# Kernel tuning notes

Measured on AMD Instinct MI355X. Metric: run time of the kernel, lower is better.

## Reference

```python
import jax, jax.numpy as jnp
import numpy as np

B, S, D = 2, 2048, 1024
H, DK, DV = 16, 64, 64
NEG = -1e9

def setup_inputs() -> dict:
    key = jax.random.key(0)
    ks = jax.random.split(key, 7)
    scale = 1.0 / np.sqrt(D)
    return {
        "Q": jax.random.normal(ks[0], (B, S, D), dtype=jnp.float32),
        "K": jax.random.normal(ks[1], (B, S, D), dtype=jnp.float32),
        "V": jax.random.normal(ks[2], (B, S, D), dtype=jnp.float32),
        "Wq": jax.random.normal(ks[3], (D, H * DK), dtype=jnp.float32) * scale,
        "Wk": jax.random.normal(ks[4], (D, H * DK), dtype=jnp.float32) * scale,
        "Wv": jax.random.normal(ks[5], (D, H * DV), dtype=jnp.float32) * scale,
        "Wo": jax.random.normal(ks[6], (H * DV, D), dtype=jnp.float32) * scale,
    }

def reference(Q, K, V, Wq, Wk, Wv, Wo):
    b, sq, _ = Q.shape
    sk = K.shape[1]
    # project and split heads: [b, h, s, d]
    q = (Q @ Wq).reshape(b, sq, H, DK).transpose(0, 2, 1, 3)
    k = (K @ Wk).reshape(b, sk, H, DK).transpose(0, 2, 1, 3)
    v = (V @ Wv).reshape(b, sk, H, DV).transpose(0, 2, 1, 3)
    scores = jnp.einsum("bhqd,bhkd->bhqk", q, k) / jnp.sqrt(jnp.float32(DK))
    causal = jnp.tril(jnp.ones((sq, sk), dtype=bool))
    scores = jnp.where(causal[None, None], scores, NEG)
    attn = jax.nn.softmax(scores, axis=-1)
    out = jnp.einsum("bhqk,bhkd->bhqd", attn, v)
    out = out.transpose(0, 2, 1, 3).reshape(b, sq, H * DV)
    return out @ Wo
```

## Files before the change

kernel.cpp:

```cpp
#include <hip/hip_runtime.h>
#include <cstdint>
#include <cstddef>


typedef __bf16 bf16x8 __attribute__((ext_vector_type(8)));
typedef __bf16 bf16x4 __attribute__((ext_vector_type(4)));
typedef float f32x4 __attribute__((ext_vector_type(4)));
typedef unsigned int u32x4 __attribute__((ext_vector_type(4)));

#define MFMA __builtin_amdgcn_mfma_f32_16x16x32_bf16

static __device__ __forceinline__ __bf16 f2b(float f) { return (__bf16)f; }

__global__ __launch_bounds__(256) void wtrans_kernel(
    const float* __restrict__ w0, const float* __restrict__ w1,
    const float* __restrict__ w2, const float* __restrict__ w3,
    __bf16* __restrict__ outT)
{
  const int z = blockIdx.z;
  const float* W = (z == 0) ? w0 : (z == 1) ? w1 : (z == 2) ? w2 : w3;
  __bf16* O = outT + (size_t)z * 1048576;
  __shared__ float t[32][33];
  const int tx = threadIdx.x & 31, ty = threadIdx.x >> 5;
  const int kb = blockIdx.y * 32, nb = blockIdx.x * 32;
#pragma unroll
  for (int i = 0; i < 4; i++)
    t[ty + i * 8][tx] = W[(size_t)(kb + ty + i * 8) * 1024 + nb + tx];
  __syncthreads();
#pragma unroll
  for (int i = 0; i < 4; i++)
    O[(size_t)(nb + ty + i * 8) * 1024 + kb + tx] = f2b(t[tx][ty + i * 8]);
}

__global__ __launch_bounds__(256) void gemm_proj_kernel(
    const float* __restrict__ A0, const float* __restrict__ A1,
    const float* __restrict__ A2, const __bf16* __restrict__ WT,
    __bf16* __restrict__ C0, __bf16* __restrict__ C1, __bf16* __restrict__ C2)
{
  const int z = blockIdx.y;
  const float* A = (z == 0) ? A0 : (z == 1) ? A1 : A2;
  const __bf16* W = WT + (size_t)z * 1048576;
  __bf16* C = (z == 0) ? C0 : (z == 1) ? C1 : C2;

  const int mt = blockIdx.x >> 3, nt = blockIdx.x & 7;
  const int mbase = mt * 128, nbase = nt * 128;

  __shared__ __align__(16) __bf16 As[128][40];
  __shared__ __align__(16) __bf16 Bs[128][40];

  const int tid = threadIdx.x;
  const int wid = tid >> 6, lane = tid & 63;
  const int wr = wid >> 1, wc = wid & 1;
  const int lr = lane & 15, kg = lane >> 4;

  f32x4 acc[4][4] = {};

  const int arow = tid >> 3, ac0 = (tid & 7) * 4;

  for (int kb = 0; kb < 32; ++kb) {
    const int k0 = kb * 32;
#pragma unroll
    for (int p = 0; p < 4; ++p) {
      const int r = arow + p * 32;
      f32x4 av = *(const f32x4*)&A[(size_t)(mbase + r) * 1024 + k0 + ac0];
      bf16x4 cv = {f2b(av[0]), f2b(av[1]), f2b(av[2]), f2b(av[3])};
      *(bf16x4*)&As[r][ac0] = cv;
    }
#pragma unroll
    for (int p = 0; p < 2; ++p) {
      const int idx = p * 256 + tid;
      const int r = idx >> 2, c8 = (idx & 3) * 8;
      *(u32x4*)&Bs[r][c8] = *(const u32x4*)&W[(size_t)(nbase + r) * 1024 + k0 + c8];
    }
    __syncthreads();

    bf16x8 af[4], bfr[4];
#pragma unroll
    for (int i = 0; i < 4; i++) af[i] = *(const bf16x8*)&As[wr * 64 + i * 16 + lr][kg * 8];
#pragma unroll
    for (int j = 0; j < 4; j++) bfr[j] = *(const bf16x8*)&Bs[wc * 64 + j * 16 + lr][kg * 8];
#pragma unroll
    for (int i = 0; i < 4; i++)
#pragma unroll
      for (int j = 0; j < 4; j++)
        acc[i][j] = MFMA(af[i], bfr[j], acc[i][j], 0, 0, 0);
    __syncthreads();
  }

  if (z == 2) {
#pragma unroll
    for (int i = 0; i < 4; i++)
#pragma unroll
      for (int j = 0; j < 4; j++) {
        const int m0 = mbase + wr * 64 + i * 16 + kg * 4;
        const int n = nbase + wc * 64 + j * 16 + lr;
        const int b = m0 >> 11, s = m0 & 2047, h = n >> 6, dv = n & 63;
        bf16x4 w;
#pragma unroll
        for (int r = 0; r < 4; r++) w[r] = f2b(acc[i][j][r]);
        *(bf16x4*)&C[(((size_t)(b * 16 + h)) * 64 + dv) * 2048 + s] = w;
      }
  } else {
#pragma unroll
    for (int i = 0; i < 4; i++)
#pragma unroll
      for (int j = 0; j < 4; j++)
#pragma unroll
        for (int r = 0; r < 4; r++) {
          const int m = mbase + wr * 64 + i * 16 + kg * 4 + r;
          const int n = nbase + wc * 64 + j * 16 + lr;
          const int b = m >> 11, s = m & 2047, h = n >> 6, dk = n & 63;
          C[(((size_t)(b * 16 + h)) * 2048 + s) * 64 + dk] = f2b(acc[i][j][r]);
        }
  }
}

__global__ __launch_bounds__(256) void attn_kernel(
    const __bf16* __restrict__ Qh, const __bf16* __restrict__ Kh,
    const __bf16* __restrict__ VTh, __bf16* __restrict__ AO)
{
  const int lin = blockIdx.y * 16 + blockIdx.x;
  const int l = (lin & 7) * 64 + (lin >> 3);
  const int xp = l & 15, bh = l >> 4;
  const int b = bh >> 4, h = bh & 15;
  const __bf16* Qp = Qh + (size_t)bh * 2048 * 64;
  const __bf16* Kp = Kh + (size_t)bh * 2048 * 64;
  const __bf16* Vp = VTh + (size_t)bh * 64 * 2048;

  __shared__ __align__(16) __bf16 Ks[2][64][72];
  __shared__ __align__(16) __bf16 Vt[2][64][72];
  __shared__ __align__(16) __bf16 Ps[4][16][72];

  const int tid = threadIdx.x, wid = tid >> 6, lane = tid & 63;
  const int lr = lane & 15, kg = lane >> 4;
  const int sr0 = tid >> 3, sc0 = (tid & 7) * 8;
  const float SCALE = 0.125f * 1.44269504f;

#pragma unroll
  for (int phase = 0; phase < 2; ++phase) {
    const int qblk = phase ? (31 - xp) : xp;
    const int qbase = qblk << 6;
    const int nkv = qblk + 1;
    const int wq = qbase + wid * 16;

    bf16x8 qf0 = *(const bf16x8*)&Qp[(size_t)(wq + lr) * 64 + kg * 8];
    bf16x8 qf1 = *(const bf16x8*)&Qp[(size_t)(wq + lr) * 64 + 32 + kg * 8];

    f32x4 ot[4] = {};
    float mrow = -1e30f, lsum = 0.f;

    u32x4 kr0 = *(const u32x4*)&Kp[(size_t)sr0 * 64 + sc0];
    u32x4 kr1 = *(const u32x4*)&Kp[(size_t)(sr0 + 32) * 64 + sc0];
    u32x4 vr0 = *(const u32x4*)&Vp[(size_t)sr0 * 2048 + sc0];
    u32x4 vr1 = *(const u32x4*)&Vp[(size_t)(sr0 + 32) * 2048 + sc0];
    __syncthreads();
    *(u32x4*)&Ks[0][sr0][sc0] = kr0;
    *(u32x4*)&Ks[0][sr0 + 32][sc0] = kr1;
    *(u32x4*)&Vt[0][sr0][sc0] = vr0;
    *(u32x4*)&Vt[0][sr0 + 32][sc0] = vr1;

    int cur = 0;
    for (int t = 0; t < nkv; ++t) {
      const int kv0 = t << 6;
      const bool pre = (t + 1 < nkv);
      if (pre) {
        const int nkv0 = kv0 + 64;
        kr0 = *(const u32x4*)&Kp[(size_t)(nkv0 + sr0) * 64 + sc0];
        kr1 = *(const u32x4*)&Kp[(size_t)(nkv0 + sr0 + 32) * 64 + sc0];
        vr0 = *(const u32x4*)&Vp[(size_t)sr0 * 2048 + nkv0 + sc0];
        vr1 = *(const u32x4*)&Vp[(size_t)(sr0 + 32) * 2048 + nkv0 + sc0];
      }
      __syncthreads();

      if (kv0 <= wq + 15) {
        f32x4 st[4] = {};
        __builtin_amdgcn_s_setprio(1);
#pragma unroll
        for (int kvt = 0; kvt < 4; ++kvt) {
          bf16x8 kf0 = *(const bf16x8*)&Ks[cur][kvt * 16 + lr][kg * 8];
          bf16x8 kf1 = *(const bf16x8*)&Ks[cur][kvt * 16 + lr][32 + kg * 8];
          st[kvt] = MFMA(kf0, qf0, st[kvt], 0, 0, 0);
          st[kvt] = MFMA(kf1, qf1, st[kvt], 0, 0, 0);
        }
        __builtin_amdgcn_s_setprio(0);

        const int qidx = wq + lr;
        const bool needmask = (kv0 + 63) > wq;
        float sv[16];
        float mx = -1e30f;
#pragma unroll
        for (int kvt = 0; kvt < 4; ++kvt)
#pragma unroll
          for (int r = 0; r < 4; ++r) {
            float v = st[kvt][r] * SCALE;
            if (needmask && (kv0 + kvt * 16 + kg * 4 + r > qidx)) v = -1e30f;
            sv[kvt * 4 + r] = v;
            mx = fmaxf(mx, v);
          }
        mx = fmaxf(mx, __shfl_xor(mx, 16));
        mx = fmaxf(mx, __shfl_xor(mx, 32));
        const float mnew = fmaxf(mrow, mx);
        const float scl = exp2f(mrow - mnew);
        mrow = mnew;
        float rs = 0.f;
#pragma unroll
        for (int kvt = 0; kvt < 4; ++kvt) {
          bf16x4 pk;
#pragma unroll
          for (int r = 0; r < 4; ++r) {
            const float p = exp2f(sv[kvt * 4 + r] - mnew);
            rs += p;
            pk[r] = f2b(p);
          }
          *(bf16x4*)&Ps[wid][lr][kvt * 16 + kg * 4] = pk;
        }
        rs += __shfl_xor(rs, 16);
        rs += __shfl_xor(rs, 32);
        lsum = lsum * scl + rs;
#pragma unroll
        for (int dvt = 0; dvt < 4; ++dvt) ot[dvt] *= scl;

#pragma unroll
        for (int h2 = 0; h2 < 2; ++h2) {
          bf16x8 pf = *(const bf16x8*)&Ps[wid][lr][h2 * 32 + kg * 8];
          __builtin_amdgcn_s_setprio(1);
#pragma unroll
          for (int dvt = 0; dvt < 4; ++dvt) {
            bf16x8 vf = *(const bf16x8*)&Vt[cur][dvt * 16 + lr][h2 * 32 + kg * 8];
            ot[dvt] = MFMA(vf, pf, ot[dvt], 0, 0, 0);
          }
          __builtin_amdgcn_s_setprio(0);
        }
      }

      if (pre) {
        const int nb = cur ^ 1;
        *(u32x4*)&Ks[nb][sr0][sc0] = kr0;
        *(u32x4*)&Ks[nb][sr0 + 32][sc0] = kr1;
        *(u32x4*)&Vt[nb][sr0][sc0] = vr0;
        *(u32x4*)&Vt[nb][sr0 + 32][sc0] = vr1;
      }
      cur ^= 1;
    }

    const float rl = 1.f / lsum;
    const int q = wq + lr;
#pragma unroll
    for (int dvt = 0; dvt < 4; ++dvt) {
      bf16x4 w;
#pragma unroll
      for (int r = 0; r < 4; ++r) w[r] = f2b(ot[dvt][r] * rl);
      *(bf16x4*)&AO[((size_t)(b * 2048 + q)) * 1024 + h * 64 + dvt * 16 + kg * 4] = w;
    }
  }
}

__global__ __launch_bounds__(256) void gemm_out_kernel(
    const __bf16* __restrict__ A, const __bf16* __restrict__ WT,
    float* __restrict__ Out)
{
  const int mt = blockIdx.x >> 3, nt = blockIdx.x & 7;
  const int mbase = mt * 128, nbase = nt * 128;

  __shared__ __align__(16) __bf16 As[128][40];
  __shared__ __align__(16) __bf16 Bs[128][40];

  const int tid = threadIdx.x;
  const int wid = tid >> 6, lane = tid & 63;
  const int wr = wid >> 1, wc = wid & 1;
  const int lr = lane & 15, kg = lane >> 4;

  f32x4 acc[4][4] = {};

  for (int kb = 0; kb < 32; ++kb) {
    const int k0 = kb * 32;
#pragma unroll
    for (int p = 0; p < 2; ++p) {
      const int idx = p * 256 + tid;
      const int r = idx >> 2, c8 = (idx & 3) * 8;
      *(u32x4*)&As[r][c8] = *(const u32x4*)&A[(size_t)(mbase + r) * 1024 + k0 + c8];
      *(u32x4*)&Bs[r][c8] = *(const u32x4*)&WT[(size_t)(nbase + r) * 1024 + k0 + c8];
    }
    __syncthreads();

    bf16x8 af[4], bfr[4];
#pragma unroll
    for (int i = 0; i < 4; i++) af[i] = *(const bf16x8*)&As[wr * 64 + i * 16 + lr][kg * 8];
#pragma unroll
    for (int j = 0; j < 4; j++) bfr[j] = *(const bf16x8*)&Bs[wc * 64 + j * 16 + lr][kg * 8];
#pragma unroll
    for (int i = 0; i < 4; i++)
#pragma unroll
      for (int j = 0; j < 4; j++)
        acc[i][j] = MFMA(af[i], bfr[j], acc[i][j], 0, 0, 0);
    __syncthreads();
  }

#pragma unroll
  for (int i = 0; i < 4; i++)
#pragma unroll
    for (int j = 0; j < 4; j++)
#pragma unroll
      for (int r = 0; r < 4; r++) {
        const int m = mbase + wr * 64 + i * 16 + kg * 4 + r;
        const int n = nbase + wc * 64 + j * 16 + lr;
        Out[(size_t)m * 1024 + n] = acc[i][j][r];
      }
}

extern "C" void kernel_launch(void* const* d_in, const int* in_sizes, int n_in,
                              void* d_out, int out_size, void* d_ws, size_t ws_size,
                              hipStream_t stream) {
  const float* Q  = (const float*)d_in[0];
  const float* K  = (const float*)d_in[1];
  const float* V  = (const float*)d_in[2];
  const float* Wq = (const float*)d_in[3];
  const float* Wk = (const float*)d_in[4];
  const float* Wv = (const float*)d_in[5];
  const float* Wo = (const float*)d_in[6];
  float* out = (float*)d_out;

  __bf16* wT  = (__bf16*)d_ws;
  __bf16* qb  = wT + (size_t)4 * 1048576;
  __bf16* kb  = qb + (size_t)4194304;
  __bf16* vtb = kb + (size_t)4194304;
  __bf16* ao  = vtb + (size_t)4194304;

  wtrans_kernel<<<dim3(32, 32, 4), 256, 0, stream>>>(Wq, Wk, Wv, Wo, wT);
  gemm_proj_kernel<<<dim3(256, 3), 256, 0, stream>>>(Q, K, V, wT, qb, kb, vtb);
  attn_kernel<<<dim3(16, 32), 256, 0, stream>>>(qb, kb, vtb, ao);
  gemm_out_kernel<<<dim3(256), 256, 0, stream>>>(ao, wT + (size_t)3 * 1048576, out);
}
```

Measured before the change: 153.3 us.

## Pre-convert activations to bf16 and use direct global-to-LDS loads in GEMMs

Adds a separate kernel that converts Q/K/V from fp32 to bf16, so the projection GEMM can stage tiles straight into LDS with global_load_lds. The same unpadded direct-to-LDS staging, with one barrier per k-step moved, is applied to the output GEMM. Both GEMMs also get a swizzled block-to-tile mapping intended to improve L2 reuse. The costs are an extra conversion pass over the activations, possible LDS bank conflicts from dropping the row padding, and a dependence on workspace size to pick the fast path.

```diff
diff --git a/kernel.cpp b/kernel.cpp
--- a/kernel.cpp
+++ b/kernel.cpp
@@ -11,6 +11,12 @@
 #define MFMA __builtin_amdgcn_mfma_f32_16x16x32_bf16
 
 static __device__ __forceinline__ __bf16 f2b(float f) { return (__bf16)f; }
+
+static __device__ __forceinline__ void gload_lds16(const void* g, void* l) {
+  __builtin_amdgcn_global_load_lds(
+      (const __attribute__((address_space(1))) void*)g,
+      (__attribute__((address_space(3))) void*)l, 16, 0, 0);
+}
 
 __global__ __launch_bounds__(256) void wtrans_kernel(
     const float* __restrict__ w0, const float* __restrict__ w1,
@@ -32,7 +38,108 @@
     O[(size_t)(nb + ty + i * 8) * 1024 + kb + tx] = f2b(t[tx][ty + i * 8]);
 }
 
-__global__ __launch_bounds__(256) void gemm_proj_kernel(
+__global__ __launch_bounds__(256) void cvt_kernel(
+    const float* __restrict__ a0, const float* __restrict__ a1,
+    const float* __restrict__ a2, __bf16* __restrict__ o0,
+    __bf16* __restrict__ o1, __bf16* __restrict__ o2)
+{
+  const int z = blockIdx.y;
+  const float* src = (z == 0) ? a0 : (z == 1) ? a1 : a2;
+  __bf16* dst = (z == 0) ? o0 : (z == 1) ? o1 : o2;
+  const int idx = blockIdx.x * 256 + threadIdx.x;
+#pragma unroll
+  for (int it = 0; it < 4; ++it) {
+    const size_t c = (size_t)(idx + it * 131072) * 8;
+    f32x4 v0 = *(const f32x4*)&src[c];
+    f32x4 v1 = *(const f32x4*)&src[c + 4];
+    bf16x8 w = {f2b(v0[0]), f2b(v0[1]), f2b(v0[2]), f2b(v0[3]),
+                f2b(v1[0]), f2b(v1[1]), f2b(v1[2]), f2b(v1[3])};
+    *(bf16x8*)&dst[c] = w;
+  }
+}
+
+__global__ __launch_bounds__(256) void gemm_proj_bf16_kernel(
+    const __bf16* __restrict__ A0, const __bf16* __restrict__ A1,
+    const __bf16* __restrict__ A2, const __bf16* __restrict__ WT,
+    __bf16* __restrict__ C0, __bf16* __restrict__ C1, __bf16* __restrict__ C2)
+{
+  const int z = blockIdx.y;
+  const __bf16* A = (z == 0) ? A0 : (z == 1) ? A1 : A2;
+  const __bf16* W = WT + (size_t)z * 1048576;
+  __bf16* C = (z == 0) ? C0 : (z == 1) ? C1 : C2;
+
+  const int bid = blockIdx.x;
+  const int t = (bid & 7) * 32 + (bid >> 3);
+  const int mt = t >> 3, nt = t & 7;
+  const int mbase = mt * 128, nbase = nt * 128;
+
+  __shared__ __align__(16) __bf16 As[128][32];
+  __shared__ __align__(16) __bf16 Bs[128][32];
+
+  const int tid = threadIdx.x;
+  const int wid = tid >> 6, lane = tid & 63;
+  const int wr = wid >> 1, wc = wid & 1;
+  const int lr = lane & 15, kg = lane >> 4;
+
+  f32x4 acc[4][4] = {};
+
+  const int srow = tid >> 2, scol = (tid & 3) * 8;
+  const int wbase = tid & 192;
+
+  for (int kb = 0; kb < 32; ++kb) {
+    const int k0 = kb * 32;
+    __syncthreads();
+#pragma unroll
+    for (int p = 0; p < 2; ++p) {
+      const int r = srow + p * 64;
+      gload_lds16(&A[(size_t)(mbase + r) * 1024 + k0 + scol],
+                  (__bf16*)As + (size_t)(p * 256 + wbase) * 8);
+      gload_lds16(&W[(size_t)(nbase + r) * 1024 + k0 + scol],
+                  (__bf16*)Bs + (size_t)(p * 256 + wbase) * 8);
+    }
+    __syncthreads();
+
+    bf16x8 af[4], bfr[4];
+#pragma unroll
+    for (int i = 0; i < 4; i++) af[i] = *(const bf16x8*)&As[wr * 64 + i * 16 + lr][kg * 8];
+#pragma unroll
+    for (int j = 0; j < 4; j++) bfr[j] = *(const bf16x8*)&Bs[wc * 64 + j * 16 + lr][kg * 8];
+#pragma unroll
+    for (int i = 0; i < 4; i++)
+#pragma unroll
+      for (int j = 0; j < 4; j++)
+        acc[i][j] = MFMA(af[i], bfr[j], acc[i][j], 0, 0, 0);
+  }
+
+  if (z == 2) {
+#pragma unroll
+    for (int i = 0; i < 4; i++)
+#pragma unroll
+      for (int j = 0; j < 4; j++) {
+        const int m0 = mbase + wr * 64 + i * 16 + kg * 4;
+        const int n = nbase + wc * 64 + j * 16 + lr;
+        const int b = m0 >> 11, s = m0 & 2047, h = n >> 6, dv = n & 63;
+        bf16x4 w;
+#pragma unroll
+        for (int r = 0; r < 4; r++) w[r] = f2b(acc[i][j][r]);
+        *(bf16x4*)&C[(((size_t)(b * 16 + h)) * 64 + dv) * 2048 + s] = w;
+      }
+  } else {
+#pragma unroll
+    for (int i = 0; i < 4; i++)
+#pragma unroll
+      for (int j = 0; j < 4; j++)
+#pragma unroll
+        for (int r = 0; r < 4; r++) {
+          const int m = mbase + wr * 64 + i * 16 + kg * 4 + r;
+          const int n = nbase + wc * 64 + j * 16 + lr;
+          const int b = m >> 11, s = m & 2047, h = n >> 6, dk = n & 63;
+          C[(((size_t)(b * 16 + h)) * 2048 + s) * 64 + dk] = f2b(acc[i][j][r]);
+        }
+  }
+}
+
+__global__ __launch_bounds__(256) void gemm_proj_f32_kernel(
     const float* __restrict__ A0, const float* __restrict__ A1,
     const float* __restrict__ A2, const __bf16* __restrict__ WT,
     __bf16* __restrict__ C0, __bf16* __restrict__ C1, __bf16* __restrict__ C2)
@@ -54,7 +161,6 @@
   const int lr = lane & 15, kg = lane >> 4;
 
   f32x4 acc[4][4] = {};
-
   const int arow = tid >> 3, ac0 = (tid & 7) * 4;
 
   for (int kb = 0; kb < 32; ++kb) {
@@ -259,11 +365,13 @@
     const __bf16* __restrict__ A, const __bf16* __restrict__ WT,
     float* __restrict__ Out)
 {
-  const int mt = blockIdx.x >> 3, nt = blockIdx.x & 7;
+  const int bid = blockIdx.x;
+  const int t = (bid & 7) * 32 + (bid >> 3);
+  const int mt = t >> 3, nt = t & 7;
   const int mbase = mt * 128, nbase = nt * 128;
 
-  __shared__ __align__(16) __bf16 As[128][40];
-  __shared__ __align__(16) __bf16 Bs[128][40];
+  __shared__ __align__(16) __bf16 As[128][32];
+  __shared__ __align__(16) __bf16 Bs[128][32];
 
   const int tid = threadIdx.x;
   const int wid = tid >> 6, lane = tid & 63;
@@ -272,14 +380,19 @@
 
   f32x4 acc[4][4] = {};
 
+  const int srow = tid >> 2, scol = (tid & 3) * 8;
+  const int wbase = tid & 192;
+
   for (int kb = 0; kb < 32; ++kb) {
     const int k0 = kb * 32;
+    __syncthreads();
 #pragma unroll
     for (int p = 0; p < 2; ++p) {
-      const int idx = p * 256 + tid;
-      const int r = idx >> 2, c8 = (idx & 3) * 8;
-      *(u32x4*)&As[r][c8] = *(const u32x4*)&A[(size_t)(mbase + r) * 1024 + k0 + c8];
-      *(u32x4*)&Bs[r][c8] = *(const u32x4*)&WT[(size_t)(nbase + r) * 1024 + k0 + c8];
+      const int r = srow + p * 64;
+      gload_lds16(&A[(size_t)(mbase + r) * 1024 + k0 + scol],
+                  (__bf16*)As + (size_t)(p * 256 + wbase) * 8);
+      gload_lds16(&WT[(size_t)(nbase + r) * 1024 + k0 + scol],
+                  (__bf16*)Bs + (size_t)(p * 256 + wbase) * 8);
     }
     __syncthreads();
 
@@ -293,7 +406,6 @@
 #pragma unroll
       for (int j = 0; j < 4; j++)
         acc[i][j] = MFMA(af[i], bfr[j], acc[i][j], 0, 0, 0);
-    __syncthreads();
   }
 
 #pragma unroll
@@ -320,14 +432,31 @@
   const float* Wo = (const float*)d_in[6];
   float* out = (float*)d_out;
 
+  const size_t M4 = 4194304;
   __bf16* wT  = (__bf16*)d_ws;
-  __bf16* qb  = wT + (size_t)4 * 1048576;
-  __bf16* kb  = qb + (size_t)4194304;
-  __bf16* vtb = kb + (size_t)4194304;
-  __bf16* ao  = vtb + (size_t)4194304;
+  __bf16* qb  = wT + M4;
+  __bf16* kb  = qb + M4;
+  __bf16* vtb = kb + M4;
+
+  const bool fast = ws_size >= (size_t)(28 * 1048576) * 2;
 
   wtrans_kernel<<<dim3(32, 32, 4), 256, 0, stream>>>(Wq, Wk, Wv, Wo, wT);
-  gemm_proj_kernel<<<dim3(256, 3), 256, 0, stream>>>(Q, K, V, wT, qb, kb, vtb);
+
+  __bf16* ao;
+  if (fast) {
+    __bf16* qa = vtb + M4;
+    __bf16* ka = qa + M4;
+    __bf16* va = ka + M4;
+    ao = qa;
+    cvt_kernel<<<dim3(512, 3), 256, 0, stream>>>(Q, K, V, qa, ka, va);
+    gemm_proj_bf16_kernel<<<dim3(256, 3), 256, 0, stream>>>(qa, ka, va, wT,
+                                                            qb, kb, vtb);
+  } else {
+    ao = vtb + M4;
+    gemm_proj_f32_kernel<<<dim3(256, 3), 256, 0, stream>>>(Q, K, V, wT,
+                                                           qb, kb, vtb);
+  }
+
   attn_kernel<<<dim3(16, 32), 256, 0, stream>>>(qb, kb, vtb, ao);
-  gemm_out_kernel<<<dim3(256), 256, 0, stream>>>(ao, wT + (size_t)3 * 1048576, out);
-}
+  gemm_out_kernel<<<dim3(256), 256, 0, stream>>>(ao, wT + 3 * 1048576, out);
+}
```

Result: faster. 137.8 us (-10.1%).
